# Optimization experiments

Hardware: AMD Instinct MI355X
Metric: run time of the kernel (lower is better)

The kernel has to match this reference:

```python
import jax, jax.numpy as jnp
import numpy as np

B, T, D, H = 2048, 200, 128, 128


def setup_inputs() -> dict:
    key = jax.random.key(0)
    k1, k2, k3, k4, k5, k6 = jax.random.split(key, 6)
    inputs = jax.random.normal(k1, (B, T, D), dtype=jnp.float32)
    att_scores = jax.random.uniform(k2, (B, T), dtype=jnp.float32)
    seq_len = jax.random.randint(k3, (B,), 0, T, dtype=jnp.int32)
    s = 1.0 / np.sqrt(D + H)
    Wg = jax.random.normal(k4, (D + H, 2 * H), dtype=jnp.float32) * s
    bg = jnp.ones((2 * H,), dtype=jnp.float32)  # TF GRU gate bias init = 1.0
    Wc = jax.random.normal(k5, (D + H, H), dtype=jnp.float32) * s
    bc = jnp.zeros((H,), dtype=jnp.float32)
    return {"inputs": inputs, "att_scores": att_scores, "seq_len": seq_len,
            "Wg": Wg, "bg": bg, "Wc": Wc, "bc": bc}


def _augru_scan(inputs, att_scores, seq_len, Wg, bg, Wc, bc):
    # time-major xs for scan
    xs = (jnp.swapaxes(inputs, 0, 1),          # [T, B, D]
          jnp.swapaxes(att_scores, 0, 1),      # [T, B]
          jnp.arange(T, dtype=jnp.int32))      # [T]
    h0 = jnp.zeros((inputs.shape[0], H), dtype=inputs.dtype)

    def step(h, x):
        x_t, a_t, t = x
        # gates: sigmoid([x, h] @ Wg + bg) -> reset r, update u
        gi = jax.nn.sigmoid(jnp.concatenate([x_t, h], axis=-1) @ Wg + bg)
        r, u = jnp.split(gi, 2, axis=-1)
        # candidate: tanh([x, r*h] @ Wc + bc)
        c = jnp.tanh(jnp.concatenate([x_t, r * h], axis=-1) @ Wc + bc)
        # attention-gated update (AUGRU): scale update gate by att score
        u = a_t[:, None] * u
        new_h = (1.0 - u) * h + u * c
        # sequence-length masking (TF _rnn_step copy_cond: time >= seq_len)
        valid = (t < seq_len)[:, None]
        out = jnp.where(valid, new_h, jnp.zeros_like(new_h))  # zero_output
        h = jnp.where(valid, new_h, h)                         # carry old state
        return h, out

    final_h, outs = jax.lax.scan(step, h0, xs)
    return jnp.swapaxes(outs, 0, 1)  # [B, T, H]


def reference(inputs, att_scores, seq_len, Wg, bg, Wc, bc):
    return _augru_scan(inputs, att_scores, seq_len, Wg, bg, Wc, bc)
```

## Files before the change

kernel.cpp:

```cpp
#include <hip/hip_runtime.h>
#include <hip/hip_bf16.h>


#define BB   2048
#define TT   200
#define DD   128
#define HH   128
#define NG   256
#define BM   8
#define SB   136
#define NTH  256

typedef __attribute__((ext_vector_type(8))) __bf16 bf16x8;
typedef __attribute__((ext_vector_type(4))) float  f32x4;

#define MFMA(a, b, c) __builtin_amdgcn_mfma_f32_16x16x32_bf16((a), (b), (c), 0, 0, 0)

union bfu { __bf16 b; unsigned short u; };
__device__ __forceinline__ unsigned short f2bf(float f) { bfu c; c.b = (__bf16)f; return c.u; }
__device__ __forceinline__ __bf16 f2bfv(float f) { return (__bf16)f; }
__device__ __forceinline__ float sigm(float x) { return __builtin_amdgcn_rcpf(1.0f + __expf(-x)); }

__device__ __forceinline__ void lds_barrier() {
    __builtin_amdgcn_sched_barrier(0);
    asm volatile("s_waitcnt lgkmcnt(0)" ::: "memory");
    __builtin_amdgcn_s_barrier();
    __builtin_amdgcn_sched_barrier(0);
}

__global__ __launch_bounds__(NTH, 1)
void augru_kernel(const float* __restrict__ X,
                  const float* __restrict__ ATT,
                  const int*   __restrict__ SL,
                  const float* __restrict__ WG,
                  const float* __restrict__ BG,
                  const float* __restrict__ WC,
                  const float* __restrict__ BC,
                  float*       __restrict__ OUT)
{
    __shared__ unsigned short xb[2][16 * SB];
    __shared__ unsigned short hb[16 * SB];
    __shared__ unsigned short rh[16 * SB];
    __shared__ float attall[BM * TT];
    __shared__ int   slbuf[BM];

    const int tid  = threadIdx.x;
    const int wave = tid >> 6;
    const int lane = tid & 63;
    const int quad = lane >> 4;
    const int l16  = lane & 15;
    const int b0   = blockIdx.x * BM;
    const int qq   = quad & 1;
    const int top  = quad >> 1;
    const int r0   = 4 * qq + 2 * top;

    for (int i = tid; i < 2 * 16 * SB; i += NTH) xb[0][i] = 0;
    for (int i = tid; i < 16 * SB; i += NTH) hb[i] = 0;
    for (int i = tid; i < 16 * SB; i += NTH) rh[i] = 0;
    for (int i = tid; i < BM * TT; i += NTH) attall[i] = ATT[(long)b0 * TT + i];
    if (tid < BM) slbuf[tid] = SL[b0 + tid];

    const int c0 = wave * 32 + l16;
    const int c1 = c0 + 16;
    const float bgr0 = BG[c0],      bgr1 = BG[c1];
    const float bgu0 = BG[c0 + HH], bgu1 = BG[c1 + HH];
    const float bc0v = BC[c0],      bc1v = BC[c1];

    bf16x8 bgf[4][8], bcf[2][8];
    {
        #pragma unroll
        for (int kk = 0; kk < 8; ++kk) {
            bf16x8 t0, t1, t2, t3, t4, t5;
            #pragma unroll
            for (int j = 0; j < 8; ++j) {
                const int k = kk * 32 + quad * 8 + j;
                t0[j] = f2bfv(WG[k * NG + c0]);
                t1[j] = f2bfv(WG[k * NG + c1]);
                t2[j] = f2bfv(WG[k * NG + c0 + HH]);
                t3[j] = f2bfv(WG[k * NG + c1 + HH]);
                t4[j] = f2bfv(WC[k * HH + c0]);
                t5[j] = f2bfv(WC[k * HH + c1]);
            }
            bgf[0][kk] = t0; bgf[1][kk] = t1; bgf[2][kk] = t2; bgf[3][kk] = t3;
            bcf[0][kk] = t4; bcf[1][kk] = t5;
        }
    }
    __syncthreads();

    int tmax = 0;
    #pragma unroll
    for (int r = 0; r < BM; ++r) tmax = max(tmax, slbuf[r]);
    const int sl0 = slbuf[r0], sl1 = slbuf[r0 + 1];

    float h00 = 0.f, h01 = 0.f, h10 = 0.f, h11 = 0.f;

    const int srow = tid >> 5;
    const int sseg = tid & 31;

    float4 xpre;
    if (tmax > 0) {
        xpre = *(const float4*)&X[((long)(b0 + srow) * TT + 0) * DD + sseg * 4];
        ushort4 v; v.x = f2bf(xpre.x); v.y = f2bf(xpre.y); v.z = f2bf(xpre.z); v.w = f2bf(xpre.w);
        *(ushort4*)&xb[0][srow * SB + sseg * 4] = v;
        if (tmax > 1)
            xpre = *(const float4*)&X[((long)(b0 + srow) * TT + 1) * DD + sseg * 4];
    }
    lds_barrier();

    for (int t = 0; t < tmax; ++t) {
        const unsigned short* xc = &xb[t & 1][0];

        bf16x8 afx[4];
        #pragma unroll
        for (int kk = 0; kk < 4; ++kk)
            afx[kk] = *(const bf16x8*)&xc[l16 * SB + kk * 32 + quad * 8];

        const float at0 = attall[r0 * TT + t];
        const float at1 = attall[(r0 + 1) * TT + t];

        f32x4 a0 = {0.f,0.f,0.f,0.f}, a1 = {0.f,0.f,0.f,0.f};
        f32x4 a2 = {0.f,0.f,0.f,0.f}, a3 = {0.f,0.f,0.f,0.f};
        f32x4 a4 = {0.f,0.f,0.f,0.f}, a5 = {0.f,0.f,0.f,0.f};
        f32x4 a6 = {0.f,0.f,0.f,0.f}, a7 = {0.f,0.f,0.f,0.f};
        a0 = MFMA(afx[0], bgf[0][0], a0); a2 = MFMA(afx[0], bgf[1][0], a2);
        a4 = MFMA(afx[0], bgf[2][0], a4); a6 = MFMA(afx[0], bgf[3][0], a6);
        a1 = MFMA(afx[1], bgf[0][1], a1); a3 = MFMA(afx[1], bgf[1][1], a3);
        a5 = MFMA(afx[1], bgf[2][1], a5); a7 = MFMA(afx[1], bgf[3][1], a7);
        a0 = MFMA(afx[2], bgf[0][2], a0); a2 = MFMA(afx[2], bgf[1][2], a2);
        a4 = MFMA(afx[2], bgf[2][2], a4); a6 = MFMA(afx[2], bgf[3][2], a6);
        a1 = MFMA(afx[3], bgf[0][3], a1); a3 = MFMA(afx[3], bgf[1][3], a3);
        a5 = MFMA(afx[3], bgf[2][3], a5); a7 = MFMA(afx[3], bgf[3][3], a7);
        {
            const bf16x8 afh0 = *(const bf16x8*)&hb[l16 * SB + 0 * 32 + quad * 8];
            const bf16x8 afh1 = *(const bf16x8*)&hb[l16 * SB + 1 * 32 + quad * 8];
            const bf16x8 afh2 = *(const bf16x8*)&hb[l16 * SB + 2 * 32 + quad * 8];
            const bf16x8 afh3 = *(const bf16x8*)&hb[l16 * SB + 3 * 32 + quad * 8];
            a0 = MFMA(afh0, bgf[0][4], a0); a2 = MFMA(afh0, bgf[1][4], a2);
            a4 = MFMA(afh0, bgf[2][4], a4); a6 = MFMA(afh0, bgf[3][4], a6);
            a1 = MFMA(afh1, bgf[0][5], a1); a3 = MFMA(afh1, bgf[1][5], a3);
            a5 = MFMA(afh1, bgf[2][5], a5); a7 = MFMA(afh1, bgf[3][5], a7);
            a0 = MFMA(afh2, bgf[0][6], a0); a2 = MFMA(afh2, bgf[1][6], a2);
            a4 = MFMA(afh2, bgf[2][6], a4); a6 = MFMA(afh2, bgf[3][6], a6);
            a1 = MFMA(afh3, bgf[0][7], a1); a3 = MFMA(afh3, bgf[1][7], a3);
            a5 = MFMA(afh3, bgf[2][7], a5); a7 = MFMA(afh3, bgf[3][7], a7);
        }

        if (t + 1 < tmax) {
            ushort4 v; v.x = f2bf(xpre.x); v.y = f2bf(xpre.y); v.z = f2bf(xpre.z); v.w = f2bf(xpre.w);
            *(ushort4*)&xb[(t + 1) & 1][srow * SB + sseg * 4] = v;
            if (t + 2 < tmax)
                xpre = *(const float4*)&X[((long)(b0 + srow) * TT + (t + 2)) * DD + sseg * 4];
        }

        const f32x4 gr0 = a0 + a1;
        const f32x4 gr1 = a2 + a3;
        const f32x4 gu0 = a4 + a5;
        const f32x4 gu1 = a6 + a7;
        const float r02 = __shfl_xor(gr0[2], 32, 64), r03 = __shfl_xor(gr0[3], 32, 64);
        const float r12 = __shfl_xor(gr1[2], 32, 64), r13 = __shfl_xor(gr1[3], 32, 64);
        const float u02 = __shfl_xor(gu0[2], 32, 64), u03 = __shfl_xor(gu0[3], 32, 64);
        const float u12 = __shfl_xor(gu1[2], 32, 64), u13 = __shfl_xor(gu1[3], 32, 64);
        float ug00, ug01, ug10, ug11;
        {
            const float rs00 = sigm((top ? r02 : gr0[0]) + bgr0);
            const float rs10 = sigm((top ? r03 : gr0[1]) + bgr0);
            rh[r0 * SB + c0]       = f2bf(rs00 * h00);
            rh[(r0 + 1) * SB + c0] = f2bf(rs10 * h10);
            ug00 = at0 * sigm((top ? u02 : gu0[0]) + bgu0);
            ug10 = at1 * sigm((top ? u03 : gu0[1]) + bgu0);
            const float rs01 = sigm((top ? r12 : gr1[0]) + bgr1);
            const float rs11 = sigm((top ? r13 : gr1[1]) + bgr1);
            rh[r0 * SB + c1]       = f2bf(rs01 * h01);
            rh[(r0 + 1) * SB + c1] = f2bf(rs11 * h11);
            ug01 = at0 * sigm((top ? u12 : gu1[0]) + bgu1);
            ug11 = at1 * sigm((top ? u13 : gu1[1]) + bgu1);
        }
        lds_barrier();

        f32x4 q0 = {0.f,0.f,0.f,0.f}, q1 = {0.f,0.f,0.f,0.f};
        f32x4 q2 = {0.f,0.f,0.f,0.f}, q3 = {0.f,0.f,0.f,0.f};
        {
            const bf16x8 afr0 = *(const bf16x8*)&rh[l16 * SB + 0 * 32 + quad * 8];
            const bf16x8 afr1 = *(const bf16x8*)&rh[l16 * SB + 1 * 32 + quad * 8];
            const bf16x8 afr2 = *(const bf16x8*)&rh[l16 * SB + 2 * 32 + quad * 8];
            const bf16x8 afr3 = *(const bf16x8*)&rh[l16 * SB + 3 * 32 + quad * 8];
            q0 = MFMA(afx[0], bcf[0][0], q0); q2 = MFMA(afx[0], bcf[1][0], q2);
            q1 = MFMA(afx[1], bcf[0][1], q1); q3 = MFMA(afx[1], bcf[1][1], q3);
            q0 = MFMA(afx[2], bcf[0][2], q0); q2 = MFMA(afx[2], bcf[1][2], q2);
            q1 = MFMA(afx[3], bcf[0][3], q1); q3 = MFMA(afx[3], bcf[1][3], q3);
            q0 = MFMA(afr0, bcf[0][4], q0);   q2 = MFMA(afr0, bcf[1][4], q2);
            q1 = MFMA(afr1, bcf[0][5], q1);   q3 = MFMA(afr1, bcf[1][5], q3);
            q0 = MFMA(afr2, bcf[0][6], q0);   q2 = MFMA(afr2, bcf[1][6], q2);
            q1 = MFMA(afr3, bcf[0][7], q1);   q3 = MFMA(afr3, bcf[1][7], q3);
        }
        const f32x4 cc0 = q0 + q1;
        const f32x4 cc1 = q2 + q3;
        const float c02 = __shfl_xor(cc0[2], 32, 64), c03 = __shfl_xor(cc0[3], 32, 64);
        const float c12 = __shfl_xor(cc1[2], 32, 64), c13 = __shfl_xor(cc1[3], 32, 64);

        {
            const bool v0 = t < sl0;
            const bool v1 = t < sl1;
            {
                const float xv = (top ? c02 : cc0[0]) + bc0v;
                const float e  = __expf(2.0f * xv);
                const float cd = 1.0f - 2.0f * __builtin_amdgcn_rcpf(e + 1.0f);
                const float nh = fmaf(ug00, cd - h00, h00);
                h00 = v0 ? nh : h00;
                hb[r0 * SB + c0] = f2bf(h00);
                OUT[((long)(b0 + r0) * TT + t) * HH + c0] = v0 ? nh : 0.f;
            }
            {
                const float xv = (top ? c03 : cc0[1]) + bc0v;
                const float e  = __expf(2.0f * xv);
                const float cd = 1.0f - 2.0f * __builtin_amdgcn_rcpf(e + 1.0f);
                const float nh = fmaf(ug10, cd - h10, h10);
                h10 = v1 ? nh : h10;
                hb[(r0 + 1) * SB + c0] = f2bf(h10);
                OUT[((long)(b0 + r0 + 1) * TT + t) * HH + c0] = v1 ? nh : 0.f;
            }
            {
                const float xv = (top ? c12 : cc1[0]) + bc1v;
                const float e  = __expf(2.0f * xv);
                const float cd = 1.0f - 2.0f * __builtin_amdgcn_rcpf(e + 1.0f);
                const float nh = fmaf(ug01, cd - h01, h01);
                h01 = v0 ? nh : h01;
                hb[r0 * SB + c1] = f2bf(h01);
                OUT[((long)(b0 + r0) * TT + t) * HH + c1] = v0 ? nh : 0.f;
            }
            {
                const float xv = (top ? c13 : cc1[1]) + bc1v;
                const float e  = __expf(2.0f * xv);
                const float cd = 1.0f - 2.0f * __builtin_amdgcn_rcpf(e + 1.0f);
                const float nh = fmaf(ug11, cd - h11, h11);
                h11 = v1 ? nh : h11;
                hb[(r0 + 1) * SB + c1] = f2bf(h11);
                OUT[((long)(b0 + r0 + 1) * TT + t) * HH + c1] = v1 ? nh : 0.f;
            }
        }
        lds_barrier();
    }

    const int n4 = (TT - tmax) * (HH / 4);
    for (int r = 0; r < BM; ++r) {
        float4* p = (float4*)(OUT + ((long)(b0 + r) * TT + tmax) * HH);
        for (int i = tid; i < n4; i += NTH) p[i] = make_float4(0.f, 0.f, 0.f, 0.f);
    }
}

extern "C" void kernel_launch(void* const* d_in, const int* in_sizes, int n_in,
                              void* d_out, int out_size, void* d_ws, size_t ws_size,
                              hipStream_t stream) {
    (void)in_sizes; (void)n_in; (void)d_ws; (void)ws_size; (void)out_size;
    const float* X   = (const float*)d_in[0];
    const float* ATT = (const float*)d_in[1];
    const int*   SL  = (const int*)d_in[2];
    const float* WG  = (const float*)d_in[3];
    const float* BG  = (const float*)d_in[4];
    const float* WC  = (const float*)d_in[5];
    const float* BC  = (const float*)d_in[6];
    float*       OUT = (float*)d_out;
    hipLaunchKernelGGL(augru_kernel, dim3(BB / BM), dim3(NTH), 0, stream,
                       X, ATT, SL, WG, BG, WC, BC, OUT);
}
```

Baseline: 501.2 us.

## Software-pipeline x-dependent gate MFMAs into previous timestep's candidate phase

The x-part of the gate GEMM for step t+1 is now issued during step t, after the candidate MFMAs and before the tanh/update epilogue. The x-part of the candidate GEMM moves ahead to run alongside the h-part of the gate GEMM. This takes input-only MFMAs off the serial recurrence critical path so they overlap with h-dependent work and with the barrier waits. In exchange it keeps more accumulator and operand registers live, which adds register pressure in a kernel already limited to one block per CU.

```diff
diff --git a/kernel.cpp b/kernel.cpp
--- a/kernel.cpp
+++ b/kernel.cpp
@@ -27,6 +27,22 @@
     __builtin_amdgcn_s_barrier();
     __builtin_amdgcn_sched_barrier(0);
 }
+
+#define GATE_X_PART(FX)                                                       \
+    a0 = MFMA(FX[0], bgf[0][0], a0); a2 = MFMA(FX[0], bgf[1][0], a2);         \
+    a4 = MFMA(FX[0], bgf[2][0], a4); a6 = MFMA(FX[0], bgf[3][0], a6);         \
+    a1 = MFMA(FX[1], bgf[0][1], a1); a3 = MFMA(FX[1], bgf[1][1], a3);         \
+    a5 = MFMA(FX[1], bgf[2][1], a5); a7 = MFMA(FX[1], bgf[3][1], a7);         \
+    a0 = MFMA(FX[2], bgf[0][2], a0); a2 = MFMA(FX[2], bgf[1][2], a2);         \
+    a4 = MFMA(FX[2], bgf[2][2], a4); a6 = MFMA(FX[2], bgf[3][2], a6);         \
+    a1 = MFMA(FX[3], bgf[0][3], a1); a3 = MFMA(FX[3], bgf[1][3], a3);         \
+    a5 = MFMA(FX[3], bgf[2][3], a5); a7 = MFMA(FX[3], bgf[3][3], a7)
+
+#define ZERO_A                                                                \
+    a0 = (f32x4){0.f,0.f,0.f,0.f}; a1 = (f32x4){0.f,0.f,0.f,0.f};             \
+    a2 = (f32x4){0.f,0.f,0.f,0.f}; a3 = (f32x4){0.f,0.f,0.f,0.f};             \
+    a4 = (f32x4){0.f,0.f,0.f,0.f}; a5 = (f32x4){0.f,0.f,0.f,0.f};             \
+    a6 = (f32x4){0.f,0.f,0.f,0.f}; a7 = (f32x4){0.f,0.f,0.f,0.f}
 
 __global__ __launch_bounds__(NTH, 1)
 void augru_kernel(const float* __restrict__ X,
@@ -97,7 +113,11 @@
     const int srow = tid >> 5;
     const int sseg = tid & 31;
 
+    f32x4 a0, a1, a2, a3, a4, a5, a6, a7;
+    ZERO_A;
+
     float4 xpre;
+    bf16x8 afx[4];
     if (tmax > 0) {
         xpre = *(const float4*)&X[((long)(b0 + srow) * TT + 0) * DD + sseg * 4];
         ushort4 v; v.x = f2bf(xpre.x); v.y = f2bf(xpre.y); v.z = f2bf(xpre.z); v.w = f2bf(xpre.w);
@@ -106,35 +126,29 @@
             xpre = *(const float4*)&X[((long)(b0 + srow) * TT + 1) * DD + sseg * 4];
     }
     lds_barrier();
-
-    for (int t = 0; t < tmax; ++t) {
-        const unsigned short* xc = &xb[t & 1][0];
-
-        bf16x8 afx[4];
+    if (tmax > 0) {
         #pragma unroll
         for (int kk = 0; kk < 4; ++kk)
-            afx[kk] = *(const bf16x8*)&xc[l16 * SB + kk * 32 + quad * 8];
+            afx[kk] = *(const bf16x8*)&xb[0][l16 * SB + kk * 32 + quad * 8];
+        GATE_X_PART(afx);
+    }
+
+    for (int t = 0; t < tmax; ++t) {
 
         const float at0 = attall[r0 * TT + t];
         const float at1 = attall[(r0 + 1) * TT + t];
 
-        f32x4 a0 = {0.f,0.f,0.f,0.f}, a1 = {0.f,0.f,0.f,0.f};
-        f32x4 a2 = {0.f,0.f,0.f,0.f}, a3 = {0.f,0.f,0.f,0.f};
-        f32x4 a4 = {0.f,0.f,0.f,0.f}, a5 = {0.f,0.f,0.f,0.f};
-        f32x4 a6 = {0.f,0.f,0.f,0.f}, a7 = {0.f,0.f,0.f,0.f};
-        a0 = MFMA(afx[0], bgf[0][0], a0); a2 = MFMA(afx[0], bgf[1][0], a2);
-        a4 = MFMA(afx[0], bgf[2][0], a4); a6 = MFMA(afx[0], bgf[3][0], a6);
-        a1 = MFMA(afx[1], bgf[0][1], a1); a3 = MFMA(afx[1], bgf[1][1], a3);
-        a5 = MFMA(afx[1], bgf[2][1], a5); a7 = MFMA(afx[1], bgf[3][1], a7);
-        a0 = MFMA(afx[2], bgf[0][2], a0); a2 = MFMA(afx[2], bgf[1][2], a2);
-        a4 = MFMA(afx[2], bgf[2][2], a4); a6 = MFMA(afx[2], bgf[3][2], a6);
-        a1 = MFMA(afx[3], bgf[0][3], a1); a3 = MFMA(afx[3], bgf[1][3], a3);
-        a5 = MFMA(afx[3], bgf[2][3], a5); a7 = MFMA(afx[3], bgf[3][3], a7);
+        f32x4 q0 = {0.f,0.f,0.f,0.f}, q1 = {0.f,0.f,0.f,0.f};
+        f32x4 q2 = {0.f,0.f,0.f,0.f}, q3 = {0.f,0.f,0.f,0.f};
         {
             const bf16x8 afh0 = *(const bf16x8*)&hb[l16 * SB + 0 * 32 + quad * 8];
             const bf16x8 afh1 = *(const bf16x8*)&hb[l16 * SB + 1 * 32 + quad * 8];
             const bf16x8 afh2 = *(const bf16x8*)&hb[l16 * SB + 2 * 32 + quad * 8];
             const bf16x8 afh3 = *(const bf16x8*)&hb[l16 * SB + 3 * 32 + quad * 8];
+            q0 = MFMA(afx[0], bcf[0][0], q0); q2 = MFMA(afx[0], bcf[1][0], q2);
+            q1 = MFMA(afx[1], bcf[0][1], q1); q3 = MFMA(afx[1], bcf[1][1], q3);
+            q0 = MFMA(afx[2], bcf[0][2], q0); q2 = MFMA(afx[2], bcf[1][2], q2);
+            q1 = MFMA(afx[3], bcf[0][3], q1); q3 = MFMA(afx[3], bcf[1][3], q3);
             a0 = MFMA(afh0, bgf[0][4], a0); a2 = MFMA(afh0, bgf[1][4], a2);
             a4 = MFMA(afh0, bgf[2][4], a4); a6 = MFMA(afh0, bgf[3][4], a6);
             a1 = MFMA(afh1, bgf[0][5], a1); a3 = MFMA(afh1, bgf[1][5], a3);
@@ -177,22 +191,27 @@
         }
         lds_barrier();
 
-        f32x4 q0 = {0.f,0.f,0.f,0.f}, q1 = {0.f,0.f,0.f,0.f};
-        f32x4 q2 = {0.f,0.f,0.f,0.f}, q3 = {0.f,0.f,0.f,0.f};
+        const bool more = (t + 1 < tmax);
+        bf16x8 afx2[4];
         {
             const bf16x8 afr0 = *(const bf16x8*)&rh[l16 * SB + 0 * 32 + quad * 8];
             const bf16x8 afr1 = *(const bf16x8*)&rh[l16 * SB + 1 * 32 + quad * 8];
             const bf16x8 afr2 = *(const bf16x8*)&rh[l16 * SB + 2 * 32 + quad * 8];
             const bf16x8 afr3 = *(const bf16x8*)&rh[l16 * SB + 3 * 32 + quad * 8];
-            q0 = MFMA(afx[0], bcf[0][0], q0); q2 = MFMA(afx[0], bcf[1][0], q2);
-            q1 = MFMA(afx[1], bcf[0][1], q1); q3 = MFMA(afx[1], bcf[1][1], q3);
-            q0 = MFMA(afx[2], bcf[0][2], q0); q2 = MFMA(afx[2], bcf[1][2], q2);
-            q1 = MFMA(afx[3], bcf[0][3], q1); q3 = MFMA(afx[3], bcf[1][3], q3);
+            if (more) {
+                const unsigned short* xn = &xb[(t + 1) & 1][0];
+                #pragma unroll
+                for (int kk = 0; kk < 4; ++kk)
+                    afx2[kk] = *(const bf16x8*)&xn[l16 * SB + kk * 32 + quad * 8];
+            }
             q0 = MFMA(afr0, bcf[0][4], q0);   q2 = MFMA(afr0, bcf[1][4], q2);
             q1 = MFMA(afr1, bcf[0][5], q1);   q3 = MFMA(afr1, bcf[1][5], q3);
             q0 = MFMA(afr2, bcf[0][6], q0);   q2 = MFMA(afr2, bcf[1][6], q2);
             q1 = MFMA(afr3, bcf[0][7], q1);   q3 = MFMA(afr3, bcf[1][7], q3);
         }
+        ZERO_A;
+        if (more) { GATE_X_PART(afx2); }
+
         const f32x4 cc0 = q0 + q1;
         const f32x4 cc1 = q2 + q3;
         const float c02 = __shfl_xor(cc0[2], 32, 64), c03 = __shfl_xor(cc0[3], 32, 64);
@@ -239,6 +258,11 @@
             }
         }
         lds_barrier();
+
+        if (more) {
+            afx[0] = afx2[0]; afx[1] = afx2[1];
+            afx[2] = afx2[2]; afx[3] = afx2[3];
+        }
     }
 
     const int n4 = (TT - tmax) * (HH / 4);
```

Measured after the change: 517.0 us. 3.2% more time.
